# Optimization experiments

Hardware: AMD Instinct MI355X
Metric: run time of the kernel (lower is better)

Reference implementation:

```python
import jax, jax.numpy as jnp
from jax import lax
import numpy as np

# model dims
N, CIN, T = 4, 1, 8000
C = 256      # encoder/bottleneck channels
D = 512      # dconv_size
K = 3        # residual kernel size
FK, FS = 20, 10  # front kernel / stride
REPEATS, BLOCKS = 4, 8
NB = REPEATS * BLOCKS
EPS = 1e-5
DN = ('NCH', 'OIH', 'NCH')


def setup_inputs() -> dict:
    key = jax.random.key(0)
    ks = jax.random.split(key, 20)
    rn = lambda k, s, sc=0.05: (jax.random.normal(k, s, dtype=jnp.float32) * sc)
    inp = {
        'x': jax.random.normal(ks[0], (N, CIN, T), dtype=jnp.float32),
        'w_enc': rn(ks[1], (C, CIN, FK), 0.2),
        'w1': rn(ks[2], (NB, D, C, 1)),
        'wd': rn(ks[3], (NB, D, 1, K), 0.2),
        'w2': rn(ks[4], (NB, C, D, 1)),
        'w_dec': rn(ks[5], (C, CIN, FK), 0.2),
    }
    # BatchNorm params (inference-style): bn1 over C, bn2/bn3 over D
    for name, ch, base in (('bn1', C, 6), ('bn2', D, 10), ('bn3', D, 14)):
        inp[name + '_g'] = 1.0 + rn(ks[base + 0], (NB, ch), 0.1)
        inp[name + '_b'] = rn(ks[base + 1], (NB, ch), 0.1)
        inp[name + '_m'] = rn(ks[base + 2], (NB, ch), 0.1)
        inp[name + '_v'] = 0.5 + jax.random.uniform(ks[base + 3], (NB, ch), dtype=jnp.float32)
    return inp


def _bn(x, g, b, m, v):
    # x: [N, C, L]; per-channel affine normalization (eval-mode BatchNorm1d)
    scale = g / jnp.sqrt(v + EPS)
    return x * scale[:, None] + (b - m * scale)[:, None]


def _conv1x1(x, w):
    # x: [N, Ci, L], w: [Co, Ci, 1]
    return jnp.einsum('ncl,oc->nol', x, w[:, :, 0])


def reference(x, w_enc, w1, wd, w2, w_dec,
              bn1_g, bn1_b, bn1_m, bn1_v,
              bn2_g, bn2_b, bn2_m, bn2_v,
              bn3_g, bn3_b, bn3_m, bn3_v):
    time = x.shape[2]
    # encoder: Conv1d(CIN->C, k=FK, stride=FS, padding=FK)
    xe = lax.conv_general_dilated(x, w_enc, (FS,), [(FK, FK)], dimension_numbers=DN)
    h = xe
    for i in range(NB):
        dil = 2 ** (i % BLOCKS)
        pad = dil * (K - 1) // 2
        r = _bn(h, bn1_g[i], bn1_b[i], bn1_m[i], bn1_v[i])
        r = _conv1x1(r, w1[i])                      # [N, D, L]
        r = _bn(r, bn2_g[i], bn2_b[i], bn2_m[i], bn2_v[i])
        r = lax.conv_general_dilated(r, wd[i], (1,), [(pad, pad)],
                                     rhs_dilation=(dil,), dimension_numbers=DN,
                                     feature_group_count=D)
        r = _bn(r, bn3_g[i], bn3_b[i], bn3_m[i], bn3_v[i])
        r = _conv1x1(r, w2[i])                      # [N, C, L]
        h = h + r
    mask = jax.nn.sigmoid(h)
    y = xe * mask
    # ConvTranspose1d(C->CIN, k=FK, stride=FS, padding=0)
    wk = jnp.flip(jnp.swapaxes(w_dec, 0, 1), -1)     # [CIN, C, FK]
    out = lax.conv_general_dilated(y, wk, (1,), [(FK - 1, FK - 1)],
                                   lhs_dilation=(FS,), dimension_numbers=DN)
    return out[:, :, FK:time + FK]
```

## Files before the change

kernel.cpp:

```cpp
#include <hip/hip_runtime.h>
#include <cstddef>
#include <cstring>

#define T_     8000
#define L_     803
#define C_     256
#define D_     512
#define NB_    32
#define FK_    20
#define NBATCH 4
#define EPS_   1e-5f

#define NVALID 208
#define NGRID  224
#define NTHR   512
#define SG     1040

typedef __attribute__((ext_vector_type(8))) short bf16x8;
typedef __attribute__((ext_vector_type(4))) short shortx4;
typedef __attribute__((ext_vector_type(4))) float f32x4;
typedef unsigned long long u64;

__device__ __forceinline__ short f2bf(float x) {
  unsigned u = __float_as_uint(x);
  u += 0x7FFF + ((u >> 16) & 1);
  return (short)(u >> 16);
}
__device__ __forceinline__ float bf2f(short u) {
  return __uint_as_float(((unsigned)(unsigned short)u) << 16);
}

__device__ __forceinline__ void astore8(void* p, u64 v) {
  __hip_atomic_store((u64*)p, v, __ATOMIC_RELAXED, __HIP_MEMORY_SCOPE_AGENT);
}

struct __align__(64) Bar { unsigned cnt; unsigned phase; unsigned pad[14]; };

__device__ __forceinline__ void bar_heavy(Bar* b, unsigned nblk, int tid) {
  __syncthreads();
  if (tid == 0) {
    __threadfence();
    unsigned ph = __hip_atomic_load(&b->phase, __ATOMIC_RELAXED, __HIP_MEMORY_SCOPE_AGENT);
    unsigned prev = __hip_atomic_fetch_add(&b->cnt, 1u, __ATOMIC_RELAXED, __HIP_MEMORY_SCOPE_AGENT);
    if (prev == nblk - 1) {
      __hip_atomic_store(&b->cnt, 0u, __ATOMIC_RELAXED, __HIP_MEMORY_SCOPE_AGENT);
      __hip_atomic_store(&b->phase, ph + 1u, __ATOMIC_RELEASE, __HIP_MEMORY_SCOPE_AGENT);
    } else {
      while (__hip_atomic_load(&b->phase, __ATOMIC_RELAXED, __HIP_MEMORY_SCOPE_AGENT) == ph)
        __builtin_amdgcn_s_sleep(2);
    }
    __threadfence();
  }
  __syncthreads();
}

struct KParams {
  const float *x, *w_enc, *w1, *wd, *w2, *w_dec;
  const float *g1, *bb1, *m1, *v1;
  const float *g2, *bb2, *m2, *v2;
  const float *g3, *bb3, *m3, *v3;
  float *out;
  float *s1, *o1, *s2, *o2, *s3, *o3;
  float *yb;
  short *w1b, *w2b;
  unsigned short *zh;
  unsigned short *b3g;
  unsigned short *b1b;
  unsigned *ct;
  Bar *gbar;
};

__global__ __launch_bounds__(256) void prep_kernel(KParams p) {
  const int gtid = blockIdx.x * 256 + threadIdx.x;
  const int stride = gridDim.x * 256;
  for (int i = gtid; i < NB_ * C_; i += stride) {
    float s = p.g1[i] * rsqrtf(p.v1[i] + EPS_);
    p.s1[i] = s; p.o1[i] = p.bb1[i] - p.m1[i] * s;
  }
  for (int i = gtid; i < NB_ * D_; i += stride) {
    float s2 = p.g2[i] * rsqrtf(p.v2[i] + EPS_);
    p.s2[i] = s2; p.o2[i] = p.bb2[i] - p.m2[i] * s2;
    float s3 = p.g3[i] * rsqrtf(p.v3[i] + EPS_);
    p.s3[i] = s3; p.o3[i] = p.bb3[i] - p.m3[i] * s3;
  }
  for (int i = gtid; i < NB_ * D_ * C_ / 4; i += stride) {
    float4 a = ((const float4*)p.w1)[i];
    float4 b = ((const float4*)p.w2)[i];
    shortx4 sa, sb;
    sa[0] = f2bf(a.x); sa[1] = f2bf(a.y); sa[2] = f2bf(a.z); sa[3] = f2bf(a.w);
    sb[0] = f2bf(b.x); sb[1] = f2bf(b.y); sb[2] = f2bf(b.z); sb[3] = f2bf(b.w);
    *(shortx4*)&p.w1b[4 * i] = sa;
    *(shortx4*)&p.w2b[4 * i] = sb;
  }
}

__global__ __launch_bounds__(NTHR) void tasnet_fused(KParams p) {
  const int tid = threadIdx.x;
  const int bid = blockIdx.x;

  const int r8 = bid & 7, t8 = bid >> 3;
  const int g = (t8 >> 2) * 8 + r8;
  const int y = t8 & 3;
  if (g >= 52) return;
  const int vid = g * 4 + y;
  const int xt = g % 13, n = g / 13;
  const int l0 = xt * 64;

  const int lane = tid & 63, wv = tid >> 6;
  const int frow = lane & 15, kg = lane >> 4;
  const int cw = wv & 3;
  const int ch = wv >> 2;
  const int cbase = y * 64 + cw * 16 + kg * 4;

  __shared__ __align__(16) char BsRaw[64 * SG];
  __shared__ __align__(16) char ZsOwn[16 * SG];

  const size_t B1B = (size_t)NBATCH * L_ * C_;
  const size_t ZHB = (size_t)52 * 4 * 64 * 128;
  const size_t B3B = (size_t)52 * 64 * 512;

  f32x4 hreg[2], xer[2];
  {
    const float* xn_ = p.x + (size_t)n * T_;
#pragma unroll
    for (int jb = 0; jb < 2; ++jb) {
      int gl = l0 + ch * 32 + jb * 16 + frow;
      int t0 = gl * 10 - 20;
      float xw[FK_];
#pragma unroll
      for (int k = 0; k < FK_; ++k) {
        int t = t0 + k;
        xw[k] = (t >= 0 && t < T_) ? xn_[t] : 0.f;
      }
#pragma unroll
      for (int jj = 0; jj < 4; ++jj) {
        const float* w = p.w_enc + (cbase + jj) * FK_;
        float acc = 0.f;
#pragma unroll
        for (int k = 0; k < FK_; ++k) acc = fmaf(xw[k], w[k], acc);
        hreg[jb][jj] = acc;
        xer[jb][jj] = acc;
      }
    }
    unsigned short* b0 = p.b1b + (size_t)n * (L_ * C_);
    float4 s1v = *(const float4*)(p.s1 + cbase);
    float4 o1v = *(const float4*)(p.o1 + cbase);
#pragma unroll
    for (int jb = 0; jb < 2; ++jb) {
      int gl = l0 + ch * 32 + jb * 16 + frow;
      if (gl < L_) {
        shortx4 pk;
        pk[0] = f2bf(fmaf(hreg[jb][0], s1v.x, o1v.x));
        pk[1] = f2bf(fmaf(hreg[jb][1], s1v.y, o1v.y));
        pk[2] = f2bf(fmaf(hreg[jb][2], s1v.z, o1v.z));
        pk[3] = f2bf(fmaf(hreg[jb][3], s1v.w, o1v.w));
        *(shortx4*)(b0 + (size_t)gl * C_ + cbase) = pk;
      }
    }
  }
  __syncthreads();
  if (tid == 0)
    __hip_atomic_store(&p.ct[vid], 1u, __ATOMIC_RELAXED, __HIP_MEMORY_SCOPE_AGENT);

  for (int layer = 0; layer < NB_; ++layer) {
    const int dil = 1 << (layer & 7);
    const int step = (dil <= 64) ? 1 : 2;
    const int w = (dil < 64) ? dil : 64;
    const float* s1p = p.s1 + layer * C_;
    const float* o1p = p.o1 + layer * C_;
    const float* s2p = p.s2 + layer * D_;
    const float* o2p = p.o2 + layer * D_;
    const float* s3p = p.s3 + layer * D_;
    const float* o3p = p.o3 + layer * D_;
    const unsigned short* b1_cur = p.b1b + (size_t)layer * B1B + (size_t)n * (L_ * C_);
    unsigned short* b1_nxt = p.b1b + (size_t)(layer + 1) * B1B + (size_t)n * (L_ * C_);
    unsigned short* zh_my = p.zh + (size_t)layer * ZHB
                            + ((size_t)(n * 13 + xt) * 4 + y) * (64 * 128);
    unsigned short* b3s = p.b3g + (size_t)(layer & 15) * B3B
                          + (size_t)(n * 13 + xt) * (64 * 512);

    {
      float4 s1v = *(const float4*)(s1p + cbase);
      float4 o1v = *(const float4*)(o1p + cbase);
#pragma unroll
      for (int jb = 0; jb < 2; ++jb) {
        int col = ch * 32 + jb * 16 + frow;
        shortx4 pk;
        pk[0] = f2bf(fmaf(hreg[jb][0], s1v.x, o1v.x));
        pk[1] = f2bf(fmaf(hreg[jb][1], s1v.y, o1v.y));
        pk[2] = f2bf(fmaf(hreg[jb][2], s1v.z, o1v.z));
        pk[3] = f2bf(fmaf(hreg[jb][3], s1v.w, o1v.w));
        *(shortx4*)(BsRaw + (cbase >> 3) * SG + col * 16 + (kg & 1) * 8) = pk;
      }
    }
    if (wv == 0 && lane < 3) {
      int idx = g * 4 + ((y + 1 + lane) & 3);
      unsigned tgt = (unsigned)(3 * layer + 1);
      while (__hip_atomic_load(&p.ct[idx], __ATOMIC_RELAXED, __HIP_MEMORY_SCOPE_AGENT) < tgt)
        __builtin_amdgcn_s_sleep(1);
    }
    __syncthreads();
    {
      int col = tid >> 3, k8 = tid & 7;
      int gl = l0 + col;
      bool lv = gl < L_;
#pragma unroll
      for (int s = 1; s < 4; ++s) {
        int sc = ((y + s) & 3) * 64 + k8 * 8;
        bf16x8 pk = {0, 0, 0, 0, 0, 0, 0, 0};
        if (lv) pk = *(const bf16x8*)(b1_cur + (size_t)gl * C_ + sc);
        *(bf16x8*)(BsRaw + (sc >> 3) * SG + col * 16) = pk;
      }
    }
    __syncthreads();

    f32x4 acc1[4] = {};
    {
      const short* W1 = p.w1b + (size_t)layer * D_ * C_ + (size_t)(y * 128 + wv * 16 + frow) * C_;
#pragma unroll
      for (int k0 = 0; k0 < 8; ++k0) {
        int kb = k0 * 32 + kg * 8;
        bf16x8 af = *(const bf16x8*)(W1 + kb);
#pragma unroll
        for (int jb = 0; jb < 4; ++jb) {
          bf16x8 bfr = *(bf16x8*)(BsRaw + (k0 * 4 + kg) * SG + (jb * 16 + frow) * 16);
          acc1[jb] = __builtin_amdgcn_mfma_f32_16x16x32_bf16(af, bfr, acc1[jb], 0, 0, 0);
        }
      }
    }
    {
      const bool hasL = (xt - step) >= 0;
      const bool hasR = (xt + step) <= 12;
      int dbr = wv * 16 + kg * 4;
      float4 s2v = *(const float4*)(s2p + y * 128 + dbr);
      float4 o2v = *(const float4*)(o2p + y * 128 + dbr);
#pragma unroll
      for (int jb = 0; jb < 4; ++jb) {
        int col = jb * 16 + frow;
        shortx4 pk;
        pk[0] = f2bf(fmaf(acc1[jb][0], s2v.x, o2v.x));
        pk[1] = f2bf(fmaf(acc1[jb][1], s2v.y, o2v.y));
        pk[2] = f2bf(fmaf(acc1[jb][2], s2v.z, o2v.z));
        pk[3] = f2bf(fmaf(acc1[jb][3], s2v.w, o2v.w));
        *(shortx4*)(ZsOwn + (dbr >> 3) * SG + col * 16 + (kg & 1) * 8) = pk;
        bool haloL = hasL && (col < w);
        bool haloR = hasR && (col >= 64 - w);
        if (haloL || haloR) {
          u64 u;
          __builtin_memcpy(&u, &pk, 8);
          astore8(zh_my + (size_t)col * 128 + dbr, u);
        }
      }
    }
    __syncthreads();
    if (tid == 0)
      __hip_atomic_store(&p.ct[vid], (unsigned)(3 * layer + 2),
                         __ATOMIC_RELAXED, __HIP_MEMORY_SCOPE_AGENT);

    {
      const int col = tid >> 3;
      const int op = tid & 7;
      const int gcol = l0 + col;
      const int gl2 = gcol - dil, gr2 = gcol + dil;
      const bool remL = (gl2 >= 0) && (gl2 < l0);
      const bool remR = (gr2 < L_) && (gr2 >= l0 + 64);
      const bool isRem = remL || remR;
      const unsigned short* zhl = p.zh + (size_t)layer * ZHB;
#pragma unroll
      for (int pass = 0; pass < 2; ++pass) {
        if (pass == 1) {
          if (wv == 0 && lane < 2) {
            int xn2 = xt + ((lane == 0) ? -step : step);
            if (xn2 >= 0 && xn2 <= 12) {
              int idx = (n * 13 + xn2) * 4 + y;
              unsigned tgt = (unsigned)(3 * layer + 2);
              while (__hip_atomic_load(&p.ct[idx], __ATOMIC_RELAXED, __HIP_MEMORY_SCOPE_AGENT) < tgt)
                __builtin_amdgcn_s_sleep(1);
            }
          }
          __syncthreads();
        }
        if ((pass == 0) == isRem) continue;
#pragma unroll
        for (int oc = 0; oc < 2; ++oc) {
          int drel = op * 16 + oc * 8;
          int dglob = y * 128 + drel;
          const float* wdp = p.wd + (size_t)layer * D_ * 3 + dglob * 3;
          float4 wq[6];
#pragma unroll
          for (int q = 0; q < 6; ++q) wq[q] = *(const float4*)(wdp + 4 * q);
          float4 s3a = *(const float4*)(s3p + dglob), s3b = *(const float4*)(s3p + dglob + 4);
          float4 o3a = *(const float4*)(o3p + dglob), o3b = *(const float4*)(o3p + dglob + 4);
          bf16x8 zc = *(bf16x8*)(ZsOwn + (drel >> 3) * SG + col * 16);
          bf16x8 zl = {0, 0, 0, 0, 0, 0, 0, 0};
          bf16x8 zr = {0, 0, 0, 0, 0, 0, 0, 0};
          if (gl2 >= 0) {
            if (!remL) zl = *(bf16x8*)(ZsOwn + (drel >> 3) * SG + (gl2 - l0) * 16);
            else zl = *(const bf16x8*)(zhl + ((size_t)(n * 13 + (gl2 >> 6)) * 4 + y) * (64 * 128)
                                       + (size_t)(gl2 & 63) * 128 + drel);
          }
          if (gr2 < L_) {
            if (!remR) zr = *(bf16x8*)(ZsOwn + (drel >> 3) * SG + (gr2 - l0) * 16);
            else zr = *(const bf16x8*)(zhl + ((size_t)(n * 13 + (gr2 >> 6)) * 4 + y) * (64 * 128)
                                       + (size_t)(gr2 & 63) * 128 + drel);
          }
          bf16x8 pb;
#pragma unroll
          for (int j = 0; j < 8; ++j) {
            float w0v = wq[(3 * j + 0) >> 2][(3 * j + 0) & 3];
            float w1v = wq[(3 * j + 1) >> 2][(3 * j + 1) & 3];
            float w2v = wq[(3 * j + 2) >> 2][(3 * j + 2) & 3];
            float m = bf2f(zc[j]) * w1v;
            m = fmaf(bf2f(zl[j]), w0v, m);
            m = fmaf(bf2f(zr[j]), w2v, m);
            float s3v = (j < 4) ? s3a[j] : s3b[j - 4];
            float o3v = (j < 4) ? o3a[j] : o3b[j - 4];
            pb[j] = f2bf(fmaf(m, s3v, o3v));
          }
          *(bf16x8*)(BsRaw + (y * 16 + (drel >> 3)) * SG + col * 16) = pb;
          *(bf16x8*)(b3s + (size_t)col * 512 + dglob) = pb;
        }
      }
    }
    __syncthreads();
    if (tid == 0)
      __hip_atomic_store(&p.ct[vid], (unsigned)(3 * layer + 3),
                         __ATOMIC_RELAXED, __HIP_MEMORY_SCOPE_AGENT);
    if (wv == 0 && lane < 3) {
      int idx = g * 4 + ((y + 1 + lane) & 3);
      unsigned tgt = (unsigned)(3 * layer + 3);
      while (__hip_atomic_load(&p.ct[idx], __ATOMIC_RELAXED, __HIP_MEMORY_SCOPE_AGENT) < tgt)
        __builtin_amdgcn_s_sleep(1);
    }
    __syncthreads();
    {
      int col = tid >> 3, k8 = tid & 7;
#pragma unroll
      for (int s = 1; s < 4; ++s) {
        int y2 = (y + s) & 3;
        const unsigned short* src = b3s + (size_t)col * 512 + y2 * 128 + k8 * 16;
        bf16x8 v0 = *(const bf16x8*)(src);
        bf16x8 v1 = *(const bf16x8*)(src + 8);
        *(bf16x8*)(BsRaw + (y2 * 16 + k8 * 2) * SG + col * 16) = v0;
        *(bf16x8*)(BsRaw + (y2 * 16 + k8 * 2 + 1) * SG + col * 16) = v1;
      }
    }
    __syncthreads();

    {
      f32x4 acc2[2] = {};
      const short* W2 = p.w2b + (size_t)layer * C_ * D_ + (size_t)(y * 64 + cw * 16 + frow) * D_;
#pragma unroll
      for (int k0 = 0; k0 < 16; ++k0) {
        int kb = k0 * 32 + kg * 8;
        bf16x8 af = *(const bf16x8*)(W2 + kb);
#pragma unroll
        for (int jb = 0; jb < 2; ++jb) {
          int col = ch * 32 + jb * 16 + frow;
          bf16x8 bfr = *(bf16x8*)(BsRaw + (k0 * 4 + kg) * SG + col * 16);
          acc2[jb] = __builtin_amdgcn_mfma_f32_16x16x32_bf16(af, bfr, acc2[jb], 0, 0, 0);
        }
      }
#pragma unroll
      for (int jb = 0; jb < 2; ++jb)
#pragma unroll
        for (int jj = 0; jj < 4; ++jj)
          hreg[jb][jj] += acc2[jb][jj];
    }
    if (layer + 1 < NB_) {
      float4 s1v = *(const float4*)(p.s1 + (layer + 1) * C_ + cbase);
      float4 o1v = *(const float4*)(p.o1 + (layer + 1) * C_ + cbase);
#pragma unroll
      for (int jb = 0; jb < 2; ++jb) {
        int gl = l0 + ch * 32 + jb * 16 + frow;
        if (gl < L_) {
          shortx4 pk;
          pk[0] = f2bf(fmaf(hreg[jb][0], s1v.x, o1v.x));
          pk[1] = f2bf(fmaf(hreg[jb][1], s1v.y, o1v.y));
          pk[2] = f2bf(fmaf(hreg[jb][2], s1v.z, o1v.z));
          pk[3] = f2bf(fmaf(hreg[jb][3], s1v.w, o1v.w));
          *(shortx4*)(b1_nxt + (size_t)gl * C_ + cbase) = pk;
        }
      }
    }
    __syncthreads();
    if (tid == 0)
      __hip_atomic_store(&p.ct[vid], (unsigned)(3 * layer + 4),
                         __ATOMIC_RELAXED, __HIP_MEMORY_SCOPE_AGENT);
  }

  {
    float* yn = p.yb + (size_t)n * ((size_t)L_ * C_);
#pragma unroll
    for (int jb = 0; jb < 2; ++jb) {
      int gl = l0 + ch * 32 + jb * 16 + frow;
      if (gl < L_) {
        float4 v;
        v.x = xer[jb][0] / (1.f + expf(-hreg[jb][0]));
        v.y = xer[jb][1] / (1.f + expf(-hreg[jb][1]));
        v.z = xer[jb][2] / (1.f + expf(-hreg[jb][2]));
        v.w = xer[jb][3] / (1.f + expf(-hreg[jb][3]));
        *(float4*)(yn + (size_t)gl * C_ + cbase) = v;
      }
    }
  }
  bar_heavy(p.gbar, NVALID, tid);

  for (int idx = vid * NTHR + tid; idx < NBATCH * T_; idx += NVALID * NTHR) {
    int t = idx % T_;
    int nn = idx / T_;
    int tt = t + FK_;
    int lq = tt / 10;
    int k0 = tt % 10;
    const float* y0 = p.yb + (size_t)nn * ((size_t)L_ * C_) + (size_t)lq * C_;
    const float* y1 = y0 - C_;
    float acc = 0.f;
#pragma unroll 8
    for (int c = 0; c < C_; c++) {
      const float* wr2 = p.w_dec + c * FK_;
      acc = fmaf(y0[c], wr2[k0], acc);
      acc = fmaf(y1[c], wr2[k0 + 10], acc);
    }
    p.out[idx] = acc;
  }
}

extern "C" void kernel_launch(void* const* d_in, const int* in_sizes, int n_in,
                              void* d_out, int out_size, void* d_ws, size_t ws_size,
                              hipStream_t stream) {
  KParams hp;
  hp.x     = (const float*)d_in[0];
  hp.w_enc = (const float*)d_in[1];
  hp.w1    = (const float*)d_in[2];
  hp.wd    = (const float*)d_in[3];
  hp.w2    = (const float*)d_in[4];
  hp.w_dec = (const float*)d_in[5];
  hp.g1 = (const float*)d_in[6];  hp.bb1 = (const float*)d_in[7];
  hp.m1 = (const float*)d_in[8];  hp.v1  = (const float*)d_in[9];
  hp.g2 = (const float*)d_in[10]; hp.bb2 = (const float*)d_in[11];
  hp.m2 = (const float*)d_in[12]; hp.v2  = (const float*)d_in[13];
  hp.g3 = (const float*)d_in[14]; hp.bb3 = (const float*)d_in[15];
  hp.m3 = (const float*)d_in[16]; hp.v3  = (const float*)d_in[17];
  hp.out = (float*)d_out;

  char* cur = (char*)d_ws;
  auto take = [&](size_t bytes) { char* r = cur; cur += (bytes + 255) & ~(size_t)255; return r; };
  hp.gbar = (Bar*)take(256);
  hp.ct   = (unsigned*)take(NVALID * 4);
  hp.s1 = (float*)take(NB_ * C_ * 4);
  hp.o1 = (float*)take(NB_ * C_ * 4);
  hp.s2 = (float*)take(NB_ * D_ * 4);
  hp.o2 = (float*)take(NB_ * D_ * 4);
  hp.s3 = (float*)take(NB_ * D_ * 4);
  hp.o3 = (float*)take(NB_ * D_ * 4);
  hp.yb  = (float*)take((size_t)NBATCH * L_ * C_ * 4);
  hp.w1b = (short*)take((size_t)NB_ * D_ * C_ * 2);
  hp.w2b = (short*)take((size_t)NB_ * D_ * C_ * 2);
  hp.b1b = (unsigned short*)take((size_t)NB_ * NBATCH * L_ * C_ * 2);
  hp.b3g = (unsigned short*)take((size_t)16 * 52 * 64 * 512 * 2);
  hp.zh  = (unsigned short*)take((size_t)NB_ * 52 * 4 * 64 * 128 * 2);

  hipMemsetAsync(d_ws, 0, 2048, stream);
  prep_kernel<<<dim3(1024), dim3(256), 0, stream>>>(hp);
  tasnet_fused<<<dim3(NGRID), dim3(NTHR), 0, stream>>>(hp);
}
```

Before: 516.2 us.

## Prefetch weight fragments into registers and overlap local GEMM2 slice with cross-block wait

W1 and W2 MFMA A-fragments are now loaded into registers early, before the barriers and spin-waits, so their global-load latency is hidden. The second GEMM is split so that its local K-slice (this block's own channel group, already in LDS) runs before waiting on peer blocks. The remaining slices run after the peer data is copied in. This raises register pressure (24 extra bf16x8 fragments) and may reduce occupancy or cause spills.

```diff
diff --git a/kernel.cpp b/kernel.cpp
--- a/kernel.cpp
+++ b/kernel.cpp
@@ -179,6 +179,15 @@
     unsigned short* b3s = p.b3g + (size_t)(layer & 15) * B3B
                           + (size_t)(n * 13 + xt) * (64 * 512);
 
+    bf16x8 w1f[8];
+    {
+      const short* W1 = p.w1b + (size_t)layer * D_ * C_
+                        + (size_t)(y * 128 + wv * 16 + frow) * C_;
+#pragma unroll
+      for (int k0 = 0; k0 < 8; ++k0)
+        w1f[k0] = *(const bf16x8*)(W1 + k0 * 32 + kg * 8);
+    }
+
     {
       float4 s1v = *(const float4*)(s1p + cbase);
       float4 o1v = *(const float4*)(o1p + cbase);
@@ -215,19 +224,26 @@
     __syncthreads();
 
     f32x4 acc1[4] = {};
-    {
-      const short* W1 = p.w1b + (size_t)layer * D_ * C_ + (size_t)(y * 128 + wv * 16 + frow) * C_;
-#pragma unroll
-      for (int k0 = 0; k0 < 8; ++k0) {
-        int kb = k0 * 32 + kg * 8;
-        bf16x8 af = *(const bf16x8*)(W1 + kb);
-#pragma unroll
-        for (int jb = 0; jb < 4; ++jb) {
-          bf16x8 bfr = *(bf16x8*)(BsRaw + (k0 * 4 + kg) * SG + (jb * 16 + frow) * 16);
-          acc1[jb] = __builtin_amdgcn_mfma_f32_16x16x32_bf16(af, bfr, acc1[jb], 0, 0, 0);
-        }
-      }
-    }
+#pragma unroll
+    for (int k0 = 0; k0 < 8; ++k0) {
+#pragma unroll
+      for (int jb = 0; jb < 4; ++jb) {
+        bf16x8 bfr = *(bf16x8*)(BsRaw + (k0 * 4 + kg) * SG + (jb * 16 + frow) * 16);
+        acc1[jb] = __builtin_amdgcn_mfma_f32_16x16x32_bf16(w1f[k0], bfr, acc1[jb], 0, 0, 0);
+      }
+    }
+
+    bf16x8 w2f[16];
+    {
+      const short* W2 = p.w2b + (size_t)layer * C_ * D_
+                        + (size_t)(y * 64 + cw * 16 + frow) * D_;
+#pragma unroll
+      for (int i = 0; i < 16; ++i) {
+        int k0 = (y * 4 + i) & 15;
+        w2f[i] = *(const bf16x8*)(W2 + k0 * 32 + kg * 8);
+      }
+    }
+
     {
       const bool hasL = (xt - step) >= 0;
       const bool hasR = (xt + step) <= 12;
@@ -326,6 +342,18 @@
     if (tid == 0)
       __hip_atomic_store(&p.ct[vid], (unsigned)(3 * layer + 3),
                          __ATOMIC_RELAXED, __HIP_MEMORY_SCOPE_AGENT);
+
+    f32x4 acc2[2] = {};
+#pragma unroll
+    for (int i = 0; i < 4; ++i) {
+      int k0 = (y * 4 + i) & 15;
+#pragma unroll
+      for (int jb = 0; jb < 2; ++jb) {
+        int col = ch * 32 + jb * 16 + frow;
+        bf16x8 bfr = *(bf16x8*)(BsRaw + (k0 * 4 + kg) * SG + col * 16);
+        acc2[jb] = __builtin_amdgcn_mfma_f32_16x16x32_bf16(w2f[i], bfr, acc2[jb], 0, 0, 0);
+      }
+    }
     if (wv == 0 && lane < 3) {
       int idx = g * 4 + ((y + 1 + lane) & 3);
       unsigned tgt = (unsigned)(3 * layer + 3);
@@ -347,26 +375,22 @@
     }
     __syncthreads();
 
-    {
-      f32x4 acc2[2] = {};
-      const short* W2 = p.w2b + (size_t)layer * C_ * D_ + (size_t)(y * 64 + cw * 16 + frow) * D_;
-#pragma unroll
-      for (int k0 = 0; k0 < 16; ++k0) {
-        int kb = k0 * 32 + kg * 8;
-        bf16x8 af = *(const bf16x8*)(W2 + kb);
-#pragma unroll
-        for (int jb = 0; jb < 2; ++jb) {
-          int col = ch * 32 + jb * 16 + frow;
-          bf16x8 bfr = *(bf16x8*)(BsRaw + (k0 * 4 + kg) * SG + col * 16);
-          acc2[jb] = __builtin_amdgcn_mfma_f32_16x16x32_bf16(af, bfr, acc2[jb], 0, 0, 0);
-        }
-      }
-#pragma unroll
-      for (int jb = 0; jb < 2; ++jb)
-#pragma unroll
-        for (int jj = 0; jj < 4; ++jj)
-          hreg[jb][jj] += acc2[jb][jj];
-    }
+#pragma unroll
+    for (int i = 4; i < 16; ++i) {
+      int k0 = (y * 4 + i) & 15;
+#pragma unroll
+      for (int jb = 0; jb < 2; ++jb) {
+        int col = ch * 32 + jb * 16 + frow;
+        bf16x8 bfr = *(bf16x8*)(BsRaw + (k0 * 4 + kg) * SG + col * 16);
+        acc2[jb] = __builtin_amdgcn_mfma_f32_16x16x32_bf16(w2f[i], bfr, acc2[jb], 0, 0, 0);
+      }
+    }
+#pragma unroll
+    for (int jb = 0; jb < 2; ++jb)
+#pragma unroll
+      for (int jj = 0; jj < 4; ++jj)
+        hreg[jb][jj] += acc2[jb][jj];
+
     if (layer + 1 < NB_) {
       float4 s1v = *(const float4*)(p.s1 + (layer + 1) * C_ + cbase);
       float4 o1v = *(const float4*)(p.o1 + (layer + 1) * C_ + cbase);
```

New measurement: 523.4 us. About the same (+1.4%).
